# Performance work log

Measured on AMD Instinct MI355X. Metric: run time of the kernel, lower is better.

Reference implementation:

```python
import jax, jax.numpy as jnp
import numpy as np


def _conv(x, w, b=None, stride=1, pad=0):
    y = jax.lax.conv_general_dilated(x, w, (stride, stride), [(pad, pad), (pad, pad)],
                                     dimension_numbers=('NCHW', 'OIHW', 'NCHW'))
    if b is not None:
        y = y + b[None, :, None, None]
    return y


def _slice3d(grid, guide):
    # Trilinear grid_sample, align_corners=False, zero padding.
    # grid: (N, C=12, D=8, GH, GW); guide: (N,1,H,W) in [-1,1]
    N, C, D, GH, GW = grid.shape
    H, W = guide.shape[2], guide.shape[3]
    xs = 2.0 * jnp.arange(W, dtype=grid.dtype) / max(W - 1, 1) - 1.0
    ys = 2.0 * jnp.arange(H, dtype=grid.dtype) / max(H - 1, 1) - 1.0
    gx = ((xs + 1.0) * GW - 1.0) * 0.5               # (W,)
    gy = ((ys + 1.0) * GH - 1.0) * 0.5               # (H,)
    gz = ((guide[:, 0] + 1.0) * D - 1.0) * 0.5       # (N,H,W)
    x0f = jnp.floor(gx); y0f = jnp.floor(gy); z0f = jnp.floor(gz)
    fx = gx - x0f; fy = gy - y0f; fz = gz - z0f
    x0 = x0f.astype(jnp.int32); y0 = y0f.astype(jnp.int32); z0 = z0f.astype(jnp.int32)
    gf = grid.reshape(N, C, D * GH * GW)

    def corner(zi, yi, xi, wz, wy, wx):
        mask = ((zi >= 0) & (zi < D)) & ((yi >= 0) & (yi < GH))[None, :, None] & ((xi >= 0) & (xi < GW))[None, None, :]
        zc = jnp.clip(zi, 0, D - 1); yc = jnp.clip(yi, 0, GH - 1); xc = jnp.clip(xi, 0, GW - 1)
        flat = zc * (GH * GW) + yc[None, :, None] * GW + xc[None, None, :]   # (N,H,W)
        v = jnp.take_along_axis(gf, flat.reshape(N, 1, H * W), axis=2).reshape(N, C, H, W)
        w = (wz * wy[None, :, None] * wx[None, None, :]) * mask.astype(grid.dtype)  # (N,H,W)
        return v * w[:, None]

    out = jnp.zeros((N, C, H, W), grid.dtype)
    for dz in (0, 1):
        for dy in (0, 1):
            for dx in (0, 1):
                out = out + corner(z0 + dz, y0 + dy, x0 + dx,
                                   fz if dz else 1.0 - fz,
                                   fy if dy else 1.0 - fy,
                                   fx if dx else 1.0 - fx)
    return out


def setup_inputs() -> dict:
    key = jax.random.key(0)
    ks = jax.random.split(key, 40)
    def w(i, shape):
        return jax.random.normal(ks[i], shape, jnp.float32) * 0.05
    return {
        'low_res': jax.random.uniform(ks[0], (4, 3, 256, 256), jnp.float32),
        'full_res': jax.random.uniform(ks[1], (4, 1, 1024, 1024), jnp.float32),
        'w0': w(2, (8, 3, 3, 3)), 'b0': w(3, (8,)),
        'w1': w(4, (16, 8, 3, 3)), 'b1': w(5, (16,)),
        'w2': w(6, (32, 16, 3, 3)), 'b2': w(7, (32,)),
        'w3': w(8, (64, 32, 3, 3)), 'b3': w(9, (64,)),
        'wl0': w(10, (64, 64, 3, 3)), 'bl0': w(11, (64,)),
        'wl1': w(12, (64, 64, 3, 3)),
        'wg1': w(13, (128, 64, 3, 3)), 'bg1': w(14, (128,)),
        'wg2': w(15, (256, 128, 3, 3)), 'bg2': w(16, (256,)),
        'wf1': w(17, (256, 448, 1, 1)), 'bf1': w(18, (256,)),
        'wf2': w(19, (128, 256, 1, 1)), 'bf2': w(20, (128,)),
        'wf3': w(21, (64, 128, 1, 1)), 'bf3': w(22, (64,)),
        'wlin': w(23, (96, 64, 1, 1)), 'blin': w(24, (96,)),
        'wgd1': w(25, (16, 1, 3, 3)), 'bgd1': w(26, (16,)),
        'wgd2': w(27, (1, 16, 1, 1)), 'bgd2': w(28, (1,)),
        'wau1': w(29, (16, 1, 1, 1)), 'bau1': w(30, (16,)),
        'wau2': w(31, (1, 16, 1, 1)), 'bau2': w(32, (1,)),
        'wav1': w(33, (16, 1, 1, 1)), 'bav1': w(34, (16,)),
        'wav2': w(35, (1, 16, 1, 1)), 'bav2': w(36, (1,)),
    }


def reference(low_res, full_res, w0, b0, w1, b1, w2, b2, w3, b3, wl0, bl0, wl1,
              wg1, bg1, wg2, bg2, wf1, bf1, wf2, bf2, wf3, bf3, wlin, blin,
              wgd1, bgd1, wgd2, bgd2, wau1, bau1, wau2, bau2, wav1, bav1, wav2, bav2):
    relu = jax.nn.relu
    N = low_res.shape[0]
    H, W = full_res.shape[2], full_res.shape[3]
    fake = jax.image.resize(low_res, (N, 3, H, W), 'bilinear')
    # splat stack: 4 stride-2 convs
    x = relu(_conv(low_res, w0, b0, 2, 1))
    x = relu(_conv(x, w1, b1, 2, 1))
    x = relu(_conv(x, w2, b2, 2, 1))
    splat = relu(_conv(x, w3, b3, 2, 1))                 # (N,64,16,16)
    local = _conv(relu(_conv(splat, wl0, bl0, 1, 1)), wl1, None, 1, 1)
    # global branch
    a0 = splat.mean(axis=(2, 3), keepdims=True)
    x1 = relu(_conv(splat, wg1, bg1, 2, 1))
    a1 = x1.mean(axis=(2, 3), keepdims=True)
    x2 = relu(_conv(x1, wg2, bg2, 2, 1))
    a2 = x2.mean(axis=(2, 3), keepdims=True)
    a = jnp.concatenate([a0, a1, a2], axis=1)            # (N,448,1,1)
    a = relu(_conv(a, wf1, bf1))
    a = relu(_conv(a, wf2, bf2))
    glob = relu(_conv(a, wf3, bf3))                      # (N,64,1,1)
    fused = relu(glob + local)
    fused = _conv(fused, wlin, blin)                     # (N,96,16,16)
    grid = fused.reshape(N, 12, 8, fused.shape[2], fused.shape[3])
    guidemap = jnp.tanh(_conv(relu(_conv(full_res, wgd1, bgd1, 1, 1)), wgd2, bgd2))
    coeff = _slice3d(grid, guidemap)                     # (N,12,H,W)
    Y = full_res * coeff[:, 3:4] + coeff[:, 0:3].sum(axis=1, keepdims=True)
    U0 = full_res * coeff[:, 7:8] + coeff[:, 4:7].sum(axis=1, keepdims=True)
    V0 = full_res * coeff[:, 11:12] + coeff[:, 8:11].sum(axis=1, keepdims=True)
    U = jnp.tanh(_conv(relu(_conv(U0, wau1, bau1)), wau2, bau2)) + fake[:, 1:2]
    V = jnp.tanh(_conv(relu(_conv(V0, wav1, bav1)), wav2, bav2)) + fake[:, 2:3]
    return jnp.concatenate([Y, U, V], axis=1)
```

## Files before the change

kernel.cpp:

```cpp
#include <hip/hip_runtime.h>
#include <math.h>


typedef float v2f __attribute__((ext_vector_type(2)));

__device__ __forceinline__ float tanh_fast(float x) {
    float e = __expf(2.0f * x);
    return 1.0f - 2.0f / (e + 1.0f);
}

template<int CIN, int COUT, int HIN, int WIN, int HOUT, int WOUT>
__global__ __launch_bounds__(256) void conv_s2_small(
    const float* __restrict__ in, const float* __restrict__ w,
    const float* __restrict__ b, float* __restrict__ out)
{
    int idx = blockIdx.x * 256 + threadIdx.x;
    int wo = idx % WOUT; int t = idx / WOUT;
    int ho = t % HOUT; t /= HOUT;
    int co = t % COUT; int n = t / COUT;
    float acc = b[co];
    int hi0 = ho * 2 - 1, wi0 = wo * 2 - 1;
    const float* wp = w + (size_t)co * CIN * 9;
    #pragma unroll
    for (int ci = 0; ci < CIN; ++ci) {
        const float* ip = in + ((size_t)(n * CIN + ci)) * HIN * WIN;
        const float* wc = wp + ci * 9;
        #pragma unroll
        for (int kh = 0; kh < 3; ++kh) {
            int hi = hi0 + kh;
            if ((unsigned)hi >= (unsigned)HIN) continue;
            const float* row = ip + hi * WIN;
            #pragma unroll
            for (int kw = 0; kw < 3; ++kw) {
                int wi = wi0 + kw;
                if ((unsigned)wi >= (unsigned)WIN) continue;
                acc = fmaf(wc[kh * 3 + kw], row[wi], acc);
            }
        }
    }
    out[idx] = fmaxf(acc, 0.0f);
}

template<int CIN, int PARTS, int STRIDE, bool RELU, bool HASB,
         int COUT, int HIN, int WIN, int HOUT, int WOUT>
__device__ __forceinline__ void conv_p_dev(
    const float* __restrict__ in, const float* __restrict__ w,
    const float* __restrict__ b, float* __restrict__ out,
    int tb, float* red)
{
    constexpr int CPT = CIN / PARTS;
    constexpr int OPB = 256 / PARTS;
    int part = threadIdx.x / OPB;
    int oidx = threadIdx.x % OPB;
    int o = tb * OPB + oidx;
    int wo = o % WOUT; int t = o / WOUT;
    int ho = t % HOUT; t /= HOUT;
    int co = t % COUT; int n = t / COUT;
    int hi0 = ho * STRIDE - 1, wi0 = wo * STRIDE - 1;
    const float* wp = w + ((size_t)co * CIN + part * CPT) * 9;
    const float* ip = in + ((size_t)n * CIN + part * CPT) * HIN * WIN;
    float acc = 0.0f;
    #pragma unroll
    for (int ci = 0; ci < CPT; ++ci) {
        const float* ic = ip + (size_t)ci * HIN * WIN;
        const float* wc = wp + ci * 9;
        #pragma unroll
        for (int kh = 0; kh < 3; ++kh) {
            int hi = hi0 + kh;
            if ((unsigned)hi >= (unsigned)HIN) continue;
            const float* row = ic + hi * WIN;
            #pragma unroll
            for (int kw = 0; kw < 3; ++kw) {
                int wi = wi0 + kw;
                if ((unsigned)wi >= (unsigned)WIN) continue;
                acc = fmaf(wc[kh * 3 + kw], row[wi], acc);
            }
        }
    }
    red[threadIdx.x] = acc;
    __syncthreads();
    if (part == 0) {
        float s = acc;
        #pragma unroll
        for (int p = 1; p < PARTS; ++p) s += red[p * OPB + oidx];
        if (HASB) s += b[co];
        if (RELU) s = fmaxf(s, 0.0f);
        out[o] = s;
    }
}

__global__ __launch_bounds__(256) void conv2_k(
    const float* __restrict__ in, const float* __restrict__ w,
    const float* __restrict__ b, float* __restrict__ out)
{
    __shared__ float red[256];
    conv_p_dev<16, 4, 2, true, true, 32, 64, 64, 32, 32>(in, w, b, out, blockIdx.x, red);
}

__global__ __launch_bounds__(256) void conv3_k(
    const float* __restrict__ in, const float* __restrict__ w,
    const float* __restrict__ b, float* __restrict__ out)
{
    __shared__ float red[256];
    conv_p_dev<32, 8, 2, true, true, 64, 32, 32, 16, 16>(in, w, b, out, blockIdx.x, red);
}

__global__ __launch_bounds__(256) void k5_l0_g1(
    const float* __restrict__ splat,
    const float* __restrict__ wl0, const float* __restrict__ bl0, float* __restrict__ l0o,
    const float* __restrict__ wg1, const float* __restrict__ bg1, float* __restrict__ x1)
{
    __shared__ float red[256];
    int bid = blockIdx.x;
    if (bid < 4096)
        conv_p_dev<64, 16, 1, true, true, 64, 16, 16, 16, 16>(splat, wl0, bl0, l0o, bid, red);
    else
        conv_p_dev<64, 16, 2, true, true, 128, 16, 16, 8, 8>(splat, wg1, bg1, x1, bid - 4096, red);
}

__global__ __launch_bounds__(256) void k6_l1_g2_means(
    const float* __restrict__ l0o, const float* __restrict__ wl1, float* __restrict__ localb,
    const float* __restrict__ x1, const float* __restrict__ wg2,
    const float* __restrict__ bg2, float* __restrict__ x2,
    const float* __restrict__ splat, float* __restrict__ avec)
{
    __shared__ float red[256];
    int bid = blockIdx.x;
    if (bid < 4096) {
        conv_p_dev<64, 16, 1, false, false, 64, 16, 16, 16, 16>(l0o, wl1, nullptr, localb, bid, red);
    } else if (bid < 5120) {
        conv_p_dev<128, 16, 2, true, true, 256, 8, 8, 4, 4>(x1, wg2, bg2, x2, bid - 4096, red);
    } else if (bid < 5184) {
        int wid = (bid - 5120) * 4 + (threadIdx.x >> 6);
        int lane = threadIdx.x & 63;
        int n = wid >> 6, c = wid & 63;
        const float* p = splat + ((size_t)(n * 64 + c)) * 256;
        float s = p[lane] + p[lane + 64] + p[lane + 128] + p[lane + 192];
        #pragma unroll
        for (int off = 32; off; off >>= 1) s += __shfl_down(s, off, 64);
        if (lane == 0) avec[n * 448 + c] = s * (1.0f / 256.0f);
    } else {
        int wid = (bid - 5184) * 4 + (threadIdx.x >> 6);
        int lane = threadIdx.x & 63;
        int n = wid >> 7, c = wid & 127;
        const float* p = x1 + ((size_t)(n * 128 + c)) * 64;
        float s = p[lane];
        #pragma unroll
        for (int off = 32; off; off >>= 1) s += __shfl_down(s, off, 64);
        if (lane == 0) avec[n * 448 + 64 + c] = s * (1.0f / 64.0f);
    }
}

__global__ __launch_bounds__(256) void fc_k(
    const float* __restrict__ avec, const float* __restrict__ x2,
    const float* __restrict__ wf1, const float* __restrict__ bf1,
    const float* __restrict__ wf2, const float* __restrict__ bf2,
    const float* __restrict__ wf3, const float* __restrict__ bf3,
    float* __restrict__ glob)
{
    __shared__ float a[448];
    __shared__ float h1[256];
    __shared__ float h2[128];
    int n = blockIdx.x, t = threadIdx.x;
    if (t < 192) a[t] = avec[n * 448 + t];
    {
        const float* p = x2 + ((size_t)(n * 256 + t)) * 16;
        float s = 0.0f;
        #pragma unroll
        for (int i = 0; i < 16; ++i) s += p[i];
        a[192 + t] = s * (1.0f / 16.0f);
    }
    __syncthreads();
    {
        float a0 = 0, a1 = 0, a2 = 0, a3 = 0;
        const float* wp = wf1 + (size_t)t * 448;
        for (int i = 0; i < 448; i += 4) {
            a0 = fmaf(wp[i], a[i], a0); a1 = fmaf(wp[i + 1], a[i + 1], a1);
            a2 = fmaf(wp[i + 2], a[i + 2], a2); a3 = fmaf(wp[i + 3], a[i + 3], a3);
        }
        float s = a0 + a1 + a2 + a3 + bf1[t];
        __syncthreads();
        h1[t] = fmaxf(s, 0.0f);
    }
    __syncthreads();
    if (t < 128) {
        float a0 = 0, a1 = 0, a2 = 0, a3 = 0;
        const float* wp = wf2 + (size_t)t * 256;
        for (int i = 0; i < 256; i += 4) {
            a0 = fmaf(wp[i], h1[i], a0); a1 = fmaf(wp[i + 1], h1[i + 1], a1);
            a2 = fmaf(wp[i + 2], h1[i + 2], a2); a3 = fmaf(wp[i + 3], h1[i + 3], a3);
        }
        h2[t] = fmaxf(a0 + a1 + a2 + a3 + bf2[t], 0.0f);
    }
    __syncthreads();
    if (t < 64) {
        float a0 = 0, a1 = 0, a2 = 0, a3 = 0;
        const float* wp = wf3 + (size_t)t * 128;
        for (int i = 0; i < 128; i += 4) {
            a0 = fmaf(wp[i], h2[i], a0); a1 = fmaf(wp[i + 1], h2[i + 1], a1);
            a2 = fmaf(wp[i + 2], h2[i + 2], a2); a3 = fmaf(wp[i + 3], h2[i + 3], a3);
        }
        glob[n * 64 + t] = fmaxf(a0 + a1 + a2 + a3 + bf3[t], 0.0f);
    }
}

__global__ __launch_bounds__(256) void fuse_grid(
    const float* __restrict__ glob, const float* __restrict__ local,
    const float* __restrict__ wlin, const float* __restrict__ blin,
    float* __restrict__ grid)
{
    int idx = blockIdx.x * 256 + threadIdx.x;
    int p = idx & 255; int k = (idx >> 8) % 96; int n = idx / (96 * 256);
    float acc = blin[k];
    const float* wp = wlin + k * 64;
    const float* gl = glob + n * 64;
    const float* lo = local + (size_t)n * 64 * 256 + p;
    #pragma unroll 8
    for (int c = 0; c < 64; ++c)
        acc = fmaf(wp[c], fmaxf(gl[c] + lo[c * 256], 0.0f), acc);
    int ch = k >> 3; int z = k & 7;
    grid[(((size_t)(n * 8 + z)) * 256 + p) * 12 + ch] = acc;
}

__global__ __launch_bounds__(256) void hdr_out_v3(
    const float* __restrict__ full, const float* __restrict__ low,
    const float* __restrict__ grid,
    const float* __restrict__ wgd1, const float* __restrict__ bgd1,
    const float* __restrict__ wgd2, const float* __restrict__ bgd2,
    const float* __restrict__ wau1, const float* __restrict__ bau1,
    const float* __restrict__ wau2, const float* __restrict__ bau2,
    const float* __restrict__ wav1, const float* __restrict__ bav1,
    const float* __restrict__ wav2, const float* __restrict__ bav2,
    float* __restrict__ out)
{
    int tid = blockIdx.x * 256 + threadIdx.x;
    int x0 = (tid & 255) << 2;
    int y = (tid >> 8) & 1023;
    int n = tid >> 18;
    const float* fp = full + ((size_t)n << 20);

    float v[3][6];
    #pragma unroll
    for (int r = 0; r < 3; ++r) {
        int yy = y + r - 1;
        bool okr = (unsigned)yy < 1024u;
        const float* row = fp + (size_t)yy * 1024;
        if (okr) {
            float4 m = *(const float4*)(row + x0);
            v[r][1] = m.x; v[r][2] = m.y; v[r][3] = m.z; v[r][4] = m.w;
            v[r][0] = (x0 > 0) ? row[x0 - 1] : 0.0f;
            v[r][5] = (x0 < 1020) ? row[x0 + 4] : 0.0f;
        } else {
            #pragma unroll
            for (int j = 0; j < 6; ++j) v[r][j] = 0.0f;
        }
    }

    float gacc[4];
    float bb = bgd2[0];
    #pragma unroll
    for (int px = 0; px < 4; ++px) gacc[px] = bb;
    #pragma unroll
    for (int k = 0; k < 16; ++k) {
        const float* wk = wgd1 + k * 9;
        float q0 = wk[0], q1 = wk[1], q2 = wk[2];
        float q3 = wk[3], q4 = wk[4], q5 = wk[5];
        float q6 = wk[6], q7 = wk[7], q8 = wk[8];
        float bk = bgd1[k], wo = wgd2[k];
        #pragma unroll
        for (int px = 0; px < 4; ++px) {
            float h = bk;
            h = fmaf(q0, v[0][px], h); h = fmaf(q1, v[0][px + 1], h); h = fmaf(q2, v[0][px + 2], h);
            h = fmaf(q3, v[1][px], h); h = fmaf(q4, v[1][px + 1], h); h = fmaf(q5, v[1][px + 2], h);
            h = fmaf(q6, v[2][px], h); h = fmaf(q7, v[2][px + 1], h); h = fmaf(q8, v[2][px + 2], h);
            gacc[px] = fmaf(wo, fmaxf(h, 0.0f), gacc[px]);
        }
    }

    float gyc = (y * (32.0f / 1023.0f) - 1.0f) * 0.5f;
    float y0f = floorf(gyc); float fy = gyc - y0f; int iy = (int)y0f;
    float wy0 = (iy >= 0 && iy < 16) ? (1.0f - fy) : 0.0f;
    float wy1 = (iy + 1 < 16) ? fy : 0.0f;
    int yi0 = min(max(iy, 0), 15), yi1 = min(iy + 1, 15);

    float sy = (y + 0.5f) * 0.25f - 0.5f;
    float syf = floorf(sy); float fyl = sy - syf;
    int jy0 = max((int)syf, 0), jy1 = min((int)syf + 1, 255);
    int jc = x0 >> 2;
    int c0 = max(jc - 1, 0), c2 = min(jc + 1, 255);
    const float* lr1 = low + ((size_t)(n * 3 + 1)) * 65536;
    const float* lr2 = low + ((size_t)(n * 3 + 2)) * 65536;
    float ua = lr1[jy0 * 256 + c0] + fyl * (lr1[jy1 * 256 + c0] - lr1[jy0 * 256 + c0]);
    float ub = lr1[jy0 * 256 + jc] + fyl * (lr1[jy1 * 256 + jc] - lr1[jy0 * 256 + jc]);
    float uc = lr1[jy0 * 256 + c2] + fyl * (lr1[jy1 * 256 + c2] - lr1[jy0 * 256 + c2]);
    float va = lr2[jy0 * 256 + c0] + fyl * (lr2[jy1 * 256 + c0] - lr2[jy0 * 256 + c0]);
    float vb = lr2[jy0 * 256 + jc] + fyl * (lr2[jy1 * 256 + jc] - lr2[jy0 * 256 + jc]);
    float vc = lr2[jy0 * 256 + c2] + fyl * (lr2[jy1 * 256 + c2] - lr2[jy0 * 256 + c2]);
    const float cfx[4] = {0.625f, 0.875f, 0.125f, 0.375f};

    const float* gbase = grid + (size_t)n * 24576;
    float Yo[4], Uo[4], Vo[4];

    #pragma unroll
    for (int px = 0; px < 4; ++px) {
        int x = x0 + px;
        float g = tanh_fast(gacc[px]);

        float gxc = (x * (32.0f / 1023.0f) - 1.0f) * 0.5f;
        float gzc = 4.0f * g + 3.5f;
        float x0f = floorf(gxc), z0f = floorf(gzc);
        float fx = gxc - x0f, fz = gzc - z0f;
        int ix = (int)x0f, iz = (int)z0f;

        float wx0 = (ix >= 0 && ix < 16) ? (1.0f - fx) : 0.0f;
        float wx1 = (ix + 1 < 16) ? fx : 0.0f;
        float wz0 = (iz >= 0 && iz < 8) ? (1.0f - fz) : 0.0f;
        float wz1 = (iz + 1 >= 0 && iz + 1 < 8) ? fz : 0.0f;
        int xi0 = min(max(ix, 0), 15), xi1 = min(ix + 1, 15);
        int zi0 = min(max(iz, 0), 7),  zi1 = min(max(iz + 1, 0), 7);

        float w00 = wy0 * wx0, w01 = wy0 * wx1, w10 = wy1 * wx0, w11 = wy1 * wx1;
        int o00 = yi0 * 16 + xi0, o01 = yi0 * 16 + xi1;
        int o10 = yi1 * 16 + xi0, o11 = yi1 * 16 + xi1;
        int z0b = zi0 * 256, z1b = zi1 * 256;

        v2f a01 = {0.f, 0.f}, a23 = {0.f, 0.f}, a45 = {0.f, 0.f};
        v2f a67 = {0.f, 0.f}, a89 = {0.f, 0.f}, aAB = {0.f, 0.f};

        #define CORNER(OFF, WK) { \
            const v2f* q = (const v2f*)(gbase + (size_t)(OFF) * 12); \
            float wk_ = (WK); v2f wv = {wk_, wk_}; \
            a01 += wv * q[0]; a23 += wv * q[1]; a45 += wv * q[2]; \
            a67 += wv * q[3]; a89 += wv * q[4]; aAB += wv * q[5]; }

        CORNER(z0b + o00, wz0 * w00)
        CORNER(z0b + o01, wz0 * w01)
        CORNER(z0b + o10, wz0 * w10)
        CORNER(z0b + o11, wz0 * w11)
        CORNER(z1b + o00, wz1 * w00)
        CORNER(z1b + o01, wz1 * w01)
        CORNER(z1b + o10, wz1 * w10)
        CORNER(z1b + o11, wz1 * w11)
        #undef CORNER

        float p = v[1][px + 1];
        float Yv = fmaf(p, a23.y, a01.x + a01.y + a23.x);
        float U0 = fmaf(p, a67.y, a45.x + a45.y + a67.x);
        float V0 = fmaf(p, aAB.y, a89.x + a89.y + aAB.x);

        v2f uv = {U0, V0};
        v2f acc2 = {bau2[0], bav2[0]};
        #pragma unroll
        for (int k = 0; k < 16; ++k) {
            v2f w1k = {wau1[k], wav1[k]};
            v2f b1k = {bau1[k], bav1[k]};
            v2f w2k = {wau2[k], wav2[k]};
            v2f h = w1k * uv + b1k;
            h.x = fmaxf(h.x, 0.0f); h.y = fmaxf(h.y, 0.0f);
            acc2 += w2k * h;
        }

        float f1 = (px < 2) ? (ua + cfx[px] * (ub - ua)) : (ub + cfx[px] * (uc - ub));
        float f2 = (px < 2) ? (va + cfx[px] * (vb - va)) : (vb + cfx[px] * (vc - vb));

        Yo[px] = Yv;
        Uo[px] = tanh_fast(acc2.x) + f1;
        Vo[px] = tanh_fast(acc2.y) + f2;
    }

    size_t base = ((size_t)n * 3) * 1048576 + (size_t)y * 1024 + x0;
    *(float4*)(out + base)            = make_float4(Yo[0], Yo[1], Yo[2], Yo[3]);
    *(float4*)(out + base + 1048576)  = make_float4(Uo[0], Uo[1], Uo[2], Uo[3]);
    *(float4*)(out + base + 2097152)  = make_float4(Vo[0], Vo[1], Vo[2], Vo[3]);
}

extern "C" void kernel_launch(void* const* d_in, const int* in_sizes, int n_in,
                              void* d_out, int out_size, void* d_ws, size_t ws_size,
                              hipStream_t stream)
{
    const float* low  = (const float*)d_in[0];
    const float* full = (const float*)d_in[1];
    const float* w0 = (const float*)d_in[2];  const float* b0 = (const float*)d_in[3];
    const float* w1 = (const float*)d_in[4];  const float* b1 = (const float*)d_in[5];
    const float* w2 = (const float*)d_in[6];  const float* b2 = (const float*)d_in[7];
    const float* w3 = (const float*)d_in[8];  const float* b3 = (const float*)d_in[9];
    const float* wl0 = (const float*)d_in[10]; const float* bl0 = (const float*)d_in[11];
    const float* wl1 = (const float*)d_in[12];
    const float* wg1 = (const float*)d_in[13]; const float* bg1 = (const float*)d_in[14];
    const float* wg2 = (const float*)d_in[15]; const float* bg2 = (const float*)d_in[16];
    const float* wf1 = (const float*)d_in[17]; const float* bf1 = (const float*)d_in[18];
    const float* wf2 = (const float*)d_in[19]; const float* bf2 = (const float*)d_in[20];
    const float* wf3 = (const float*)d_in[21]; const float* bf3 = (const float*)d_in[22];
    const float* wlin = (const float*)d_in[23]; const float* blin = (const float*)d_in[24];
    const float* wgd1 = (const float*)d_in[25]; const float* bgd1 = (const float*)d_in[26];
    const float* wgd2 = (const float*)d_in[27]; const float* bgd2 = (const float*)d_in[28];
    const float* wau1 = (const float*)d_in[29]; const float* bau1 = (const float*)d_in[30];
    const float* wau2 = (const float*)d_in[31]; const float* bau2 = (const float*)d_in[32];
    const float* wav1 = (const float*)d_in[33]; const float* bav1 = (const float*)d_in[34];
    const float* wav2 = (const float*)d_in[35]; const float* bav2 = (const float*)d_in[36];
    float* out = (float*)d_out;

    float* ws = (float*)d_ws;
    float* t0b    = ws;
    float* t1b    = t0b + 524288;
    float* t2b    = t1b + 262144;
    float* splat  = t2b + 131072;
    float* l0o    = splat + 65536;
    float* localb = l0o + 65536;
    float* x1b    = localb + 65536;
    float* x2b    = x1b + 32768;
    float* avec   = x2b + 16384;
    float* glob   = avec + 1792;
    float* gridb  = glob + 256;

    conv_s2_small<3, 8, 256, 256, 128, 128><<<2048, 256, 0, stream>>>(low, w0, b0, t0b);
    conv_s2_small<8, 16, 128, 128, 64, 64><<<1024, 256, 0, stream>>>(t0b, w1, b1, t1b);
    conv2_k<<<2048, 256, 0, stream>>>(t1b, w2, b2, t2b);
    conv3_k<<<2048, 256, 0, stream>>>(t2b, w3, b3, splat);
    k5_l0_g1<<<6144, 256, 0, stream>>>(splat, wl0, bl0, l0o, wg1, bg1, x1b);
    k6_l1_g2_means<<<5312, 256, 0, stream>>>(l0o, wl1, localb, x1b, wg2, bg2, x2b, splat, avec);
    fc_k<<<4, 256, 0, stream>>>(avec, x2b, wf1, bf1, wf2, bf2, wf3, bf3, glob);
    fuse_grid<<<384, 256, 0, stream>>>(glob, localb, wlin, blin, gridb);
    hdr_out_v3<<<4096, 256, 0, stream>>>(full, low, gridb,
        wgd1, bgd1, wgd2, bgd2, wau1, bau1, wau2, bau2, wav1, bav1, wav2, bav2, out);
}
```

Before: 395.0 us.

## Fuse FC head into grid kernel, move splat means, revert hdr kernel to v2 form

Moves the splat channel mean into the k5 launch and fuses the FC MLP with the grid projection, so each of 384 blocks recomputes the global vector and one launch plus the glob buffer are removed. The output kernel drops its packed v2f arithmetic and per-row hoisting of the grid y-weights and low-res upsampling, and recomputes these per pixel with scalar code. This trades fewer launches for redundant FC work and more per-pixel arithmetic and loads in the hot kernel.

```diff
diff --git a/kernel.cpp b/kernel.cpp
--- a/kernel.cpp
+++ b/kernel.cpp
@@ -1,8 +1,6 @@
 #include <hip/hip_runtime.h>
 #include <math.h>
 
-
-typedef float v2f __attribute__((ext_vector_type(2)));
 
 __device__ __forceinline__ float tanh_fast(float x) {
     float e = __expf(2.0f * x);
@@ -105,24 +103,35 @@
     conv_p_dev<32, 8, 2, true, true, 64, 32, 32, 16, 16>(in, w, b, out, blockIdx.x, red);
 }
 
-__global__ __launch_bounds__(256) void k5_l0_g1(
+__global__ __launch_bounds__(256) void k5_l0_g1_means(
     const float* __restrict__ splat,
     const float* __restrict__ wl0, const float* __restrict__ bl0, float* __restrict__ l0o,
-    const float* __restrict__ wg1, const float* __restrict__ bg1, float* __restrict__ x1)
+    const float* __restrict__ wg1, const float* __restrict__ bg1, float* __restrict__ x1,
+    float* __restrict__ avec)
 {
     __shared__ float red[256];
     int bid = blockIdx.x;
-    if (bid < 4096)
+    if (bid < 4096) {
         conv_p_dev<64, 16, 1, true, true, 64, 16, 16, 16, 16>(splat, wl0, bl0, l0o, bid, red);
-    else
+    } else if (bid < 6144) {
         conv_p_dev<64, 16, 2, true, true, 128, 16, 16, 8, 8>(splat, wg1, bg1, x1, bid - 4096, red);
+    } else {
+        int wid = (bid - 6144) * 4 + (threadIdx.x >> 6);
+        int lane = threadIdx.x & 63;
+        int n = wid >> 6, c = wid & 63;
+        const float* p = splat + ((size_t)(n * 64 + c)) * 256;
+        float s = p[lane] + p[lane + 64] + p[lane + 128] + p[lane + 192];
+        #pragma unroll
+        for (int off = 32; off; off >>= 1) s += __shfl_down(s, off, 64);
+        if (lane == 0) avec[n * 448 + c] = s * (1.0f / 256.0f);
+    }
 }
 
 __global__ __launch_bounds__(256) void k6_l1_g2_means(
     const float* __restrict__ l0o, const float* __restrict__ wl1, float* __restrict__ localb,
     const float* __restrict__ x1, const float* __restrict__ wg2,
     const float* __restrict__ bg2, float* __restrict__ x2,
-    const float* __restrict__ splat, float* __restrict__ avec)
+    float* __restrict__ avec)
 {
     __shared__ float red[256];
     int bid = blockIdx.x;
@@ -130,17 +139,8 @@
         conv_p_dev<64, 16, 1, false, false, 64, 16, 16, 16, 16>(l0o, wl1, nullptr, localb, bid, red);
     } else if (bid < 5120) {
         conv_p_dev<128, 16, 2, true, true, 256, 8, 8, 4, 4>(x1, wg2, bg2, x2, bid - 4096, red);
-    } else if (bid < 5184) {
+    } else {
         int wid = (bid - 5120) * 4 + (threadIdx.x >> 6);
-        int lane = threadIdx.x & 63;
-        int n = wid >> 6, c = wid & 63;
-        const float* p = splat + ((size_t)(n * 64 + c)) * 256;
-        float s = p[lane] + p[lane + 64] + p[lane + 128] + p[lane + 192];
-        #pragma unroll
-        for (int off = 32; off; off >>= 1) s += __shfl_down(s, off, 64);
-        if (lane == 0) avec[n * 448 + c] = s * (1.0f / 256.0f);
-    } else {
-        int wid = (bid - 5184) * 4 + (threadIdx.x >> 6);
         int lane = threadIdx.x & 63;
         int n = wid >> 7, c = wid & 127;
         const float* p = x1 + ((size_t)(n * 128 + c)) * 64;
@@ -151,17 +151,20 @@
     }
 }
 
-__global__ __launch_bounds__(256) void fc_k(
+__global__ __launch_bounds__(256) void kfc_fuse(
     const float* __restrict__ avec, const float* __restrict__ x2,
     const float* __restrict__ wf1, const float* __restrict__ bf1,
     const float* __restrict__ wf2, const float* __restrict__ bf2,
     const float* __restrict__ wf3, const float* __restrict__ bf3,
-    float* __restrict__ glob)
+    const float* __restrict__ local,
+    const float* __restrict__ wlin, const float* __restrict__ blin,
+    float* __restrict__ grid)
 {
     __shared__ float a[448];
     __shared__ float h1[256];
     __shared__ float h2[128];
-    int n = blockIdx.x, t = threadIdx.x;
+    __shared__ float gl[64];
+    int n = blockIdx.x / 96; int k = blockIdx.x % 96; int t = threadIdx.x;
     if (t < 192) a[t] = avec[n * 448 + t];
     {
         const float* p = x2 + ((size_t)(n * 256 + t)) * 16;
@@ -178,9 +181,7 @@
             a0 = fmaf(wp[i], a[i], a0); a1 = fmaf(wp[i + 1], a[i + 1], a1);
             a2 = fmaf(wp[i + 2], a[i + 2], a2); a3 = fmaf(wp[i + 3], a[i + 3], a3);
         }
-        float s = a0 + a1 + a2 + a3 + bf1[t];
-        __syncthreads();
-        h1[t] = fmaxf(s, 0.0f);
+        h1[t] = fmaxf(a0 + a1 + a2 + a3 + bf1[t], 0.0f);
     }
     __syncthreads();
     if (t < 128) {
@@ -200,29 +201,20 @@
             a0 = fmaf(wp[i], h2[i], a0); a1 = fmaf(wp[i + 1], h2[i + 1], a1);
             a2 = fmaf(wp[i + 2], h2[i + 2], a2); a3 = fmaf(wp[i + 3], h2[i + 3], a3);
         }
-        glob[n * 64 + t] = fmaxf(a0 + a1 + a2 + a3 + bf3[t], 0.0f);
-    }
-}
-
-__global__ __launch_bounds__(256) void fuse_grid(
-    const float* __restrict__ glob, const float* __restrict__ local,
-    const float* __restrict__ wlin, const float* __restrict__ blin,
-    float* __restrict__ grid)
-{
-    int idx = blockIdx.x * 256 + threadIdx.x;
-    int p = idx & 255; int k = (idx >> 8) % 96; int n = idx / (96 * 256);
+        gl[t] = fmaxf(a0 + a1 + a2 + a3 + bf3[t], 0.0f);
+    }
+    __syncthreads();
     float acc = blin[k];
     const float* wp = wlin + k * 64;
-    const float* gl = glob + n * 64;
-    const float* lo = local + (size_t)n * 64 * 256 + p;
+    const float* lo = local + (size_t)n * 64 * 256 + t;
     #pragma unroll 8
     for (int c = 0; c < 64; ++c)
         acc = fmaf(wp[c], fmaxf(gl[c] + lo[c * 256], 0.0f), acc);
     int ch = k >> 3; int z = k & 7;
-    grid[(((size_t)(n * 8 + z)) * 256 + p) * 12 + ch] = acc;
-}
-
-__global__ __launch_bounds__(256) void hdr_out_v3(
+    grid[(((size_t)(n * 8 + z)) * 256 + t) * 12 + ch] = acc;
+}
+
+__global__ __launch_bounds__(256) void hdr_out_v2(
     const float* __restrict__ full, const float* __restrict__ low,
     const float* __restrict__ grid,
     const float* __restrict__ wgd1, const float* __restrict__ bgd1,
@@ -277,27 +269,6 @@
         }
     }
 
-    float gyc = (y * (32.0f / 1023.0f) - 1.0f) * 0.5f;
-    float y0f = floorf(gyc); float fy = gyc - y0f; int iy = (int)y0f;
-    float wy0 = (iy >= 0 && iy < 16) ? (1.0f - fy) : 0.0f;
-    float wy1 = (iy + 1 < 16) ? fy : 0.0f;
-    int yi0 = min(max(iy, 0), 15), yi1 = min(iy + 1, 15);
-
-    float sy = (y + 0.5f) * 0.25f - 0.5f;
-    float syf = floorf(sy); float fyl = sy - syf;
-    int jy0 = max((int)syf, 0), jy1 = min((int)syf + 1, 255);
-    int jc = x0 >> 2;
-    int c0 = max(jc - 1, 0), c2 = min(jc + 1, 255);
-    const float* lr1 = low + ((size_t)(n * 3 + 1)) * 65536;
-    const float* lr2 = low + ((size_t)(n * 3 + 2)) * 65536;
-    float ua = lr1[jy0 * 256 + c0] + fyl * (lr1[jy1 * 256 + c0] - lr1[jy0 * 256 + c0]);
-    float ub = lr1[jy0 * 256 + jc] + fyl * (lr1[jy1 * 256 + jc] - lr1[jy0 * 256 + jc]);
-    float uc = lr1[jy0 * 256 + c2] + fyl * (lr1[jy1 * 256 + c2] - lr1[jy0 * 256 + c2]);
-    float va = lr2[jy0 * 256 + c0] + fyl * (lr2[jy1 * 256 + c0] - lr2[jy0 * 256 + c0]);
-    float vb = lr2[jy0 * 256 + jc] + fyl * (lr2[jy1 * 256 + jc] - lr2[jy0 * 256 + jc]);
-    float vc = lr2[jy0 * 256 + c2] + fyl * (lr2[jy1 * 256 + c2] - lr2[jy0 * 256 + c2]);
-    const float cfx[4] = {0.625f, 0.875f, 0.125f, 0.375f};
-
     const float* gbase = grid + (size_t)n * 24576;
     float Yo[4], Uo[4], Vo[4];
 
@@ -307,16 +278,20 @@
         float g = tanh_fast(gacc[px]);
 
         float gxc = (x * (32.0f / 1023.0f) - 1.0f) * 0.5f;
+        float gyc = (y * (32.0f / 1023.0f) - 1.0f) * 0.5f;
         float gzc = 4.0f * g + 3.5f;
-        float x0f = floorf(gxc), z0f = floorf(gzc);
-        float fx = gxc - x0f, fz = gzc - z0f;
-        int ix = (int)x0f, iz = (int)z0f;
+        float x0f = floorf(gxc), y0f = floorf(gyc), z0f = floorf(gzc);
+        float fx = gxc - x0f, fy = gyc - y0f, fz = gzc - z0f;
+        int ix = (int)x0f, iy = (int)y0f, iz = (int)z0f;
 
         float wx0 = (ix >= 0 && ix < 16) ? (1.0f - fx) : 0.0f;
         float wx1 = (ix + 1 < 16) ? fx : 0.0f;
+        float wy0 = (iy >= 0 && iy < 16) ? (1.0f - fy) : 0.0f;
+        float wy1 = (iy + 1 < 16) ? fy : 0.0f;
         float wz0 = (iz >= 0 && iz < 8) ? (1.0f - fz) : 0.0f;
         float wz1 = (iz + 1 >= 0 && iz + 1 < 8) ? fz : 0.0f;
         int xi0 = min(max(ix, 0), 15), xi1 = min(ix + 1, 15);
+        int yi0 = min(max(iy, 0), 15), yi1 = min(iy + 1, 15);
         int zi0 = min(max(iz, 0), 7),  zi1 = min(max(iz + 1, 0), 7);
 
         float w00 = wy0 * wx0, w01 = wy0 * wx1, w10 = wy1 * wx0, w11 = wy1 * wx1;
@@ -324,14 +299,20 @@
         int o10 = yi1 * 16 + xi0, o11 = yi1 * 16 + xi1;
         int z0b = zi0 * 256, z1b = zi1 * 256;
 
-        v2f a01 = {0.f, 0.f}, a23 = {0.f, 0.f}, a45 = {0.f, 0.f};
-        v2f a67 = {0.f, 0.f}, a89 = {0.f, 0.f}, aAB = {0.f, 0.f};
+        float acc[12];
+        #pragma unroll
+        for (int i = 0; i < 12; ++i) acc[i] = 0.0f;
 
         #define CORNER(OFF, WK) { \
-            const v2f* q = (const v2f*)(gbase + (size_t)(OFF) * 12); \
-            float wk_ = (WK); v2f wv = {wk_, wk_}; \
-            a01 += wv * q[0]; a23 += wv * q[1]; a45 += wv * q[2]; \
-            a67 += wv * q[3]; a89 += wv * q[4]; aAB += wv * q[5]; }
+            const float4* q = (const float4*)(gbase + (size_t)(OFF) * 12); \
+            float wk_ = (WK); \
+            float4 A = q[0], B = q[1], C = q[2]; \
+            acc[0] = fmaf(wk_, A.x, acc[0]); acc[1] = fmaf(wk_, A.y, acc[1]); \
+            acc[2] = fmaf(wk_, A.z, acc[2]); acc[3] = fmaf(wk_, A.w, acc[3]); \
+            acc[4] = fmaf(wk_, B.x, acc[4]); acc[5] = fmaf(wk_, B.y, acc[5]); \
+            acc[6] = fmaf(wk_, B.z, acc[6]); acc[7] = fmaf(wk_, B.w, acc[7]); \
+            acc[8] = fmaf(wk_, C.x, acc[8]); acc[9] = fmaf(wk_, C.y, acc[9]); \
+            acc[10] = fmaf(wk_, C.z, acc[10]); acc[11] = fmaf(wk_, C.w, acc[11]); }
 
         CORNER(z0b + o00, wz0 * w00)
         CORNER(z0b + o01, wz0 * w01)
@@ -344,28 +325,35 @@
         #undef CORNER
 
         float p = v[1][px + 1];
-        float Yv = fmaf(p, a23.y, a01.x + a01.y + a23.x);
-        float U0 = fmaf(p, a67.y, a45.x + a45.y + a67.x);
-        float V0 = fmaf(p, aAB.y, a89.x + a89.y + aAB.x);
-
-        v2f uv = {U0, V0};
-        v2f acc2 = {bau2[0], bav2[0]};
-        #pragma unroll
-        for (int k = 0; k < 16; ++k) {
-            v2f w1k = {wau1[k], wav1[k]};
-            v2f b1k = {bau1[k], bav1[k]};
-            v2f w2k = {wau2[k], wav2[k]};
-            v2f h = w1k * uv + b1k;
-            h.x = fmaxf(h.x, 0.0f); h.y = fmaxf(h.y, 0.0f);
-            acc2 += w2k * h;
-        }
-
-        float f1 = (px < 2) ? (ua + cfx[px] * (ub - ua)) : (ub + cfx[px] * (uc - ub));
-        float f2 = (px < 2) ? (va + cfx[px] * (vb - va)) : (vb + cfx[px] * (vc - vb));
+        float Yv = fmaf(p, acc[3],  acc[0] + acc[1] + acc[2]);
+        float U0 = fmaf(p, acc[7],  acc[4] + acc[5] + acc[6]);
+        float V0 = fmaf(p, acc[11], acc[8] + acc[9] + acc[10]);
+
+        float uacc = bau2[0];
+        #pragma unroll
+        for (int k = 0; k < 16; ++k)
+            uacc = fmaf(wau2[k], fmaxf(fmaf(wau1[k], U0, bau1[k]), 0.0f), uacc);
+        float vacc = bav2[0];
+        #pragma unroll
+        for (int k = 0; k < 16; ++k)
+            vacc = fmaf(wav2[k], fmaxf(fmaf(wav1[k], V0, bav1[k]), 0.0f), vacc);
+
+        float sx = (x + 0.5f) * 0.25f - 0.5f;
+        float sy = (y + 0.5f) * 0.25f - 0.5f;
+        float sxf = floorf(sx), syf = floorf(sy);
+        float fxl = sx - sxf, fyl = sy - syf;
+        int jx0 = max((int)sxf, 0), jx1 = min((int)sxf + 1, 255);
+        int jy0 = max((int)syf, 0), jy1 = min((int)syf + 1, 255);
+        const float* lr1 = low + ((size_t)(n * 3 + 1)) * 65536;
+        const float* lr2 = low + ((size_t)(n * 3 + 2)) * 65536;
+        float f1 = (1.0f - fyl) * ((1.0f - fxl) * lr1[jy0 * 256 + jx0] + fxl * lr1[jy0 * 256 + jx1])
+                 + fyl * ((1.0f - fxl) * lr1[jy1 * 256 + jx0] + fxl * lr1[jy1 * 256 + jx1]);
+        float f2 = (1.0f - fyl) * ((1.0f - fxl) * lr2[jy0 * 256 + jx0] + fxl * lr2[jy0 * 256 + jx1])
+                 + fyl * ((1.0f - fxl) * lr2[jy1 * 256 + jx0] + fxl * lr2[jy1 * 256 + jx1]);
 
         Yo[px] = Yv;
-        Uo[px] = tanh_fast(acc2.x) + f1;
-        Vo[px] = tanh_fast(acc2.y) + f2;
+        Uo[px] = tanh_fast(uacc) + f1;
+        Vo[px] = tanh_fast(vacc) + f2;
     }
 
     size_t base = ((size_t)n * 3) * 1048576 + (size_t)y * 1024 + x0;
@@ -410,17 +398,16 @@
     float* x1b    = localb + 65536;
     float* x2b    = x1b + 32768;
     float* avec   = x2b + 16384;
-    float* glob   = avec + 1792;
-    float* gridb  = glob + 256;
+    float* gridb  = avec + 1792;
 
     conv_s2_small<3, 8, 256, 256, 128, 128><<<2048, 256, 0, stream>>>(low, w0, b0, t0b);
     conv_s2_small<8, 16, 128, 128, 64, 64><<<1024, 256, 0, stream>>>(t0b, w1, b1, t1b);
     conv2_k<<<2048, 256, 0, stream>>>(t1b, w2, b2, t2b);
     conv3_k<<<2048, 256, 0, stream>>>(t2b, w3, b3, splat);
-    k5_l0_g1<<<6144, 256, 0, stream>>>(splat, wl0, bl0, l0o, wg1, bg1, x1b);
-    k6_l1_g2_means<<<5312, 256, 0, stream>>>(l0o, wl1, localb, x1b, wg2, bg2, x2b, splat, avec);
-    fc_k<<<4, 256, 0, stream>>>(avec, x2b, wf1, bf1, wf2, bf2, wf3, bf3, glob);
-    fuse_grid<<<384, 256, 0, stream>>>(glob, localb, wlin, blin, gridb);
-    hdr_out_v3<<<4096, 256, 0, stream>>>(full, low, gridb,
+    k5_l0_g1_means<<<6208, 256, 0, stream>>>(splat, wl0, bl0, l0o, wg1, bg1, x1b, avec);
+    k6_l1_g2_means<<<5248, 256, 0, stream>>>(l0o, wl1, localb, x1b, wg2, bg2, x2b, avec);
+    kfc_fuse<<<384, 256, 0, stream>>>(avec, x2b, wf1, bf1, wf2, bf2, wf3, bf3,
+                                      localb, wlin, blin, gridb);
+    hdr_out_v2<<<4096, 256, 0, stream>>>(full, low, gridb,
         wgd1, bgd1, wgd2, bgd2, wau1, bau1, wau2, bau2, wav1, bav1, wav2, bav2, out);
 }
```

After: 362.7 us. 1.09x faster.
